# Kernel optimization log

Measured on AMD Instinct MI355X. Metric: run time of the kernel, lower is better.

## Reference

```python
import jax, jax.numpy as jnp
import numpy as np

B, S, E, H = 8, 1024, 1024, 16
D = E // H  # 64
HALF = D // 2  # 32


def _apply_rope(t, freqs):
    # t: (B, S, H, D), freqs: (S, HALF)
    emb = jnp.concatenate([freqs, freqs], axis=-1)  # (S, D)
    cos = jnp.cos(emb)[None, :, None, :]  # (1, S, 1, D)
    sin = jnp.sin(emb)[None, :, None, :]
    t1, t2 = t[..., :D // 2], t[..., D // 2:]
    rot = jnp.concatenate([-t2, t1], axis=-1)
    return t * cos + rot * sin


def setup_inputs() -> dict:
    key = jax.random.key(0)
    ks = jax.random.split(key, 10)
    std = 1.0 / np.sqrt(E)
    return {
        "hidden_states": jax.random.normal(ks[0], (B, S, E), jnp.float32),
        "rotary_pos_emb": jax.random.uniform(ks[1], (S, HALF), jnp.float32) * 10.0,
        "wq": jax.random.normal(ks[2], (E, E), jnp.float32) * std,
        "bq": jnp.zeros((E,), jnp.float32),
        "wk": jax.random.normal(ks[3], (E, E), jnp.float32) * std,
        "bk": jnp.zeros((E,), jnp.float32),
        "wv": jax.random.normal(ks[4], (E, E), jnp.float32) * std,
        "bv": jnp.zeros((E,), jnp.float32),
        "wo": jax.random.normal(ks[5], (E, E), jnp.float32) * std,
        "bo": jnp.zeros((E,), jnp.float32),
    }


def reference(hidden_states, rotary_pos_emb, wq, bq, wk, bk, wv, bv, wo, bo):
    b, s, e = hidden_states.shape
    # QKV projections -> (B, S, H, D)
    q = (hidden_states @ wq + bq).reshape(b, s, H, D)
    k = (hidden_states @ wk + bk).reshape(b, s, H, D)
    v = (hidden_states @ wv + bv).reshape(b, s, H, D)
    # rotary embedding (computed in fp32, matching the torch code)
    q = _apply_rope(q.astype(jnp.float32), rotary_pos_emb).astype(hidden_states.dtype)
    k = _apply_rope(k.astype(jnp.float32), rotary_pos_emb).astype(hidden_states.dtype)
    scale = 1.0 / np.sqrt(D)
    # attention scores (B, H, Sq, Sk)
    scores = jnp.einsum("bqhd,bkhd->bhqk", q, k) * scale
    attn = jax.nn.softmax(scores, axis=-1)
    out = jnp.einsum("bhqk,bkhd->bqhd", attn, v).reshape(b, s, e)
    return out @ wo + bo
```

## Files before the change

kernel.cpp:

```cpp
#include <hip/hip_runtime.h>
#include <hip/hip_bf16.h>

typedef __hip_bfloat16 bf16;
typedef __attribute__((ext_vector_type(8))) short bfrag;
typedef __attribute__((ext_vector_type(4))) float f32x4;

#define MFMA(a, b, c) __builtin_amdgcn_mfma_f32_16x16x32_bf16((a), (b), (c), 0, 0, 0)

__device__ __forceinline__ void async16(const void* g, void* l) {
  __builtin_amdgcn_global_load_lds(
      (const __attribute__((address_space(1))) unsigned int*)g,
      (__attribute__((address_space(3))) unsigned int*)l, 16, 0, 0);
}

__device__ __forceinline__ bfrag ldfrag(const bf16* p) { return *(const bfrag*)p; }

__device__ __forceinline__ unsigned short f2b(float f) {
  return __hip_bfloat16_raw(__float2bfloat16(f)).x;
}
__device__ __forceinline__ float b2f(short u) {
  __hip_bfloat16_raw r; r.x = (unsigned short)u;
  return __bfloat162float(__hip_bfloat16(r));
}

__device__ __forceinline__ bfrag scale8(bfrag x) {
  bfrag y;
#pragma unroll
  for (int i = 0; i < 8; i++) y[i] = (short)f2b(b2f(x[i]) * 0.125f);
  return y;
}

__device__ __forceinline__ void pack4_store(bf16* p, f32x4 v, float s) {
  union { unsigned short h[4]; uint2 u; } pk;
#pragma unroll
  for (int i = 0; i < 4; i++) pk.h[i] = f2b(v[i] * s);
  *(uint2*)p = pk.u;
}


__global__ void k_tables(const float* __restrict__ rp, float* __restrict__ ctab,
                         float* __restrict__ stab) {
  int i = blockIdx.x * 256 + threadIdx.x;
  float f = rp[i];
  ctab[i] = cosf(f);
  stab[i] = sinf(f);
}

__global__ void k_convert_x(const float* __restrict__ X, unsigned short* __restrict__ Xb) {
  int i = blockIdx.x * 256 + threadIdx.x;
  float4 v = *(const float4*)(X + (size_t)i * 4);
  union { unsigned short h[4]; uint2 u; } pk;
  pk.h[0] = f2b(v.x); pk.h[1] = f2b(v.y); pk.h[2] = f2b(v.z); pk.h[3] = f2b(v.w);
  *(uint2*)(Xb + (size_t)i * 4) = pk.u;
}

__global__ void k_transpose_w(const float* __restrict__ wq, const float* __restrict__ wk,
                              const float* __restrict__ wv, const float* __restrict__ wo,
                              unsigned short* __restrict__ tq, unsigned short* __restrict__ tk,
                              unsigned short* __restrict__ tv, unsigned short* __restrict__ to) {
  const int z = blockIdx.z;
  const float* src = (z == 0) ? wq : (z == 1) ? wk : (z == 2) ? wv : wo;
  unsigned short* dst = (z == 0) ? tq : (z == 1) ? tk : (z == 2) ? tv : to;
  const int cc = blockIdx.x * 256 + threadIdx.x;
  const int r0 = blockIdx.y * 8;
  union { unsigned short h[8]; uint4 u; } pk;
#pragma unroll
  for (int i = 0; i < 8; i++) pk.h[i] = f2b(src[(r0 + i) * 1024 + cc]);
  *(uint4*)(dst + cc * 1024 + r0) = pk.u;
}


template <bool ROPE, bool F32OUT, bool BIAS_ROW, int CSTRIDE>
__device__ __forceinline__ void gemm_core(int m0, int n0, const bf16* __restrict__ A,
                                          const bf16* __restrict__ BT,
                                          const float* __restrict__ bias,
                                          bf16* __restrict__ C, float* __restrict__ Cf,
                                          const float* __restrict__ ctab,
                                          const float* __restrict__ stab) {
  __shared__ __align__(16) bf16 As[128 * 32];
  __shared__ __align__(16) bf16 Bs[128 * 32];
  const int tid = threadIdx.x;
  const int w = tid >> 6, l = tid & 63;
  const int wm = (w >> 1) << 6, wn = (w & 1) << 6;
  const int c = l & 15, quad = l >> 4;

  f32x4 acc[4][4] = {};

  const int srow = (w * 2) * 16 + (l >> 2);
  const int scol = (l & 3) * 8;
  const bf16* gA0 = A + (size_t)(m0 + srow) * 1024 + scol;
  const bf16* gA1 = gA0 + 16 * 1024;
  const bf16* gB0 = BT + (size_t)(n0 + srow) * 1024 + scol;
  const bf16* gB1 = gB0 + 16 * 1024;
  char* lA0 = (char*)As + (w * 2) * 1024;
  char* lB0 = (char*)Bs + (w * 2) * 1024;

  for (int k0 = 0; k0 < 1024; k0 += 32) {
    __syncthreads();
    async16(gA0 + k0, lA0);
    async16(gA1 + k0, lA0 + 1024);
    async16(gB0 + k0, lB0);
    async16(gB1 + k0, lB0 + 1024);
    __syncthreads();
    bfrag a[4], b[4];
#pragma unroll
    for (int i = 0; i < 4; i++) a[i] = ldfrag(&As[(wm + i * 16 + c) * 32 + quad * 8]);
#pragma unroll
    for (int j = 0; j < 4; j++) b[j] = ldfrag(&Bs[(wn + j * 16 + c) * 32 + quad * 8]);
#pragma unroll
    for (int i = 0; i < 4; i++)
#pragma unroll
      for (int j = 0; j < 4; j++) acc[i][j] = MFMA(a[i], b[j], acc[i][j]);
  }

#pragma unroll
  for (int i = 0; i < 4; i++) {
    const int mb = m0 + wm + i * 16 + quad * 4;
    if (!ROPE) {
      float brow[4];
      if (BIAS_ROW) {
#pragma unroll
        for (int r = 0; r < 4; r++) brow[r] = bias[mb + r];
      }
#pragma unroll
      for (int j = 0; j < 4; j++) {
        const int n = n0 + wn + j * 16 + c;
        const float bcol = BIAS_ROW ? 0.0f : bias[n];
#pragma unroll
        for (int r = 0; r < 4; r++) {
          const float val = acc[i][j][r] + (BIAS_ROW ? brow[r] : bcol);
          if (F32OUT)
            Cf[(size_t)(mb + r) * CSTRIDE + n] = val;
          else
            C[(size_t)(mb + r) * CSTRIDE + n] = __float2bfloat16(val);
        }
      }
    } else {
#pragma unroll
      for (int j = 0; j < 2; j++) {
        const int n1 = n0 + wn + j * 16 + c;
        const int n2 = n1 + 32;
        const int dl = j * 16 + c;
        const float b1 = bias[n1];
        const float b2 = bias[n2];
#pragma unroll
        for (int r = 0; r < 4; r++) {
          const int m = mb + r;
          const int s = m & 1023;
          const float cs = ctab[s * 32 + dl];
          const float sn = stab[s * 32 + dl];
          const float t1 = acc[i][j][r] + b1;
          const float t2 = acc[i][j + 2][r] + b2;
          C[(size_t)m * CSTRIDE + n1] = __float2bfloat16(t1 * cs - t2 * sn);
          C[(size_t)m * CSTRIDE + n2] = __float2bfloat16(t2 * cs + t1 * sn);
        }
      }
    }
  }
}

__global__ __launch_bounds__(256) void k_gemm_qkv(
    const bf16* __restrict__ X, const bf16* __restrict__ wqT, const bf16* __restrict__ wkT,
    const bf16* __restrict__ wvT, const float* __restrict__ bq, const float* __restrict__ bk,
    const float* __restrict__ bv, const float* __restrict__ ctab,
    const float* __restrict__ stab, bf16* __restrict__ Q, bf16* __restrict__ Kb,
    bf16* __restrict__ VT) {
  const int z = blockIdx.z;
  if (z == 0)
    gemm_core<true, false, false, 1024>(blockIdx.x * 128, blockIdx.y * 128, X, wqT, bq, Q,
                                        nullptr, ctab, stab);
  else if (z == 1)
    gemm_core<true, false, false, 1024>(blockIdx.x * 128, blockIdx.y * 128, X, wkT, bk, Kb,
                                        nullptr, ctab, stab);
  else
    gemm_core<false, false, true, 8192>(blockIdx.y * 128, blockIdx.x * 128, wvT, X, bv, VT,
                                        nullptr, nullptr, nullptr);
}

__global__ __launch_bounds__(256) void k_gemm_o(const bf16* __restrict__ A,
                                                const bf16* __restrict__ BT,
                                                const float* __restrict__ bias,
                                                float* __restrict__ Cf) {
  gemm_core<false, true, false, 1024>(blockIdx.x * 128, blockIdx.y * 128, A, BT, bias,
                                      nullptr, Cf, nullptr, nullptr);
}


__global__ __launch_bounds__(256, 4) void k_flash(const bf16* __restrict__ Q,
                                                  const bf16* __restrict__ K,
                                                  const bf16* __restrict__ VT,
                                                  bf16* __restrict__ O) {
  __shared__ __align__(16) bf16 Ks[64 * 64];
  __shared__ __align__(16) bf16 Vs[64 * 64];
  __shared__ __align__(16) bf16 Ps[4][32 * 72];
  const int qt = blockIdx.x, bh = blockIdx.y;
  const int b = bh >> 4, h = bh & 15;
  const int tid = threadIdx.x, w = tid >> 6, l = tid & 63;
  const int c = l & 15, quad = l >> 4;
  const int c7 = c & 7;

  bfrag qf[2][2];
#pragma unroll
  for (int qs = 0; qs < 2; qs++) {
    const bf16* qp =
        Q + (size_t)(b * 1024 + qt * 128 + w * 32 + qs * 16 + c) * 1024 + h * 64 + quad * 8;
    qf[qs][0] = scale8(ldfrag(qp));
    qf[qs][1] = scale8(ldfrag(qp + 32));
  }

  bfrag onesf;
#pragma unroll
  for (int i = 0; i < 8; i++) onesf[i] = (short)0x3F80;

  f32x4 oacc[2][4] = {};
  f32x4 lacc[2] = {};

  const int sr = l >> 3, scc = l & 7;
  const int swz = (scc ^ sr) * 8;
  const bf16* gK0 = K + (size_t)(b * 1024 + w * 16 + sr) * 1024 + h * 64 + swz;
  const bf16* gV0 = VT + (size_t)(h * 64 + w * 16 + sr) * 8192 + b * 1024 + swz;
  char* lK = (char*)Ks + w * 2048;
  char* lV = (char*)Vs + w * 2048;
  bf16* psw = Ps[w];

  for (int kt = 0; kt < 16; kt++) {
    __syncthreads();
    async16(gK0 + (size_t)(kt * 64) * 1024, lK);
    async16(gK0 + (size_t)(kt * 64 + 8) * 1024, lK + 1024);
    async16(gV0 + kt * 64, lV);
    async16(gV0 + 8 * 8192 + kt * 64, lV + 1024);
    __syncthreads();

#pragma unroll
    for (int qs = 0; qs < 2; qs++) {
      f32x4 sacc[4] = {};
#pragma unroll
      for (int mj = 0; mj < 4; mj++) {
        bfrag k0 = ldfrag(&Ks[(mj * 16 + c) * 64 + (quad ^ c7) * 8]);
        bfrag k1 = ldfrag(&Ks[(mj * 16 + c) * 64 + ((quad + 4) ^ c7) * 8]);
        sacc[mj] = MFMA(k0, qf[qs][0], sacc[mj]);
        sacc[mj] = MFMA(k1, qf[qs][1], sacc[mj]);
      }
      const int psrow = (qs * 16 + c) * 72;
#pragma unroll
      for (int mj = 0; mj < 4; mj++) {
        f32x4 p;
#pragma unroll
        for (int r = 0; r < 4; r++) p[r] = __expf(sacc[mj][r]);
        pack4_store(&psw[psrow + mj * 16 + quad * 4], p, 1.0f);
      }
    }

    bfrag pf[2][2];
#pragma unroll
    for (int qs = 0; qs < 2; qs++) {
      pf[qs][0] = ldfrag(&psw[(qs * 16 + c) * 72 + quad * 8]);
      pf[qs][1] = ldfrag(&psw[(qs * 16 + c) * 72 + 32 + quad * 8]);
      lacc[qs] = MFMA(onesf, pf[qs][0], lacc[qs]);
      lacc[qs] = MFMA(onesf, pf[qs][1], lacc[qs]);
    }
#pragma unroll
    for (int dj = 0; dj < 4; dj++) {
      bfrag v0 = ldfrag(&Vs[(dj * 16 + c) * 64 + (quad ^ c7) * 8]);
      bfrag v1 = ldfrag(&Vs[(dj * 16 + c) * 64 + ((quad + 4) ^ c7) * 8]);
#pragma unroll
      for (int qs = 0; qs < 2; qs++) {
        oacc[qs][dj] = MFMA(v0, pf[qs][0], oacc[qs][dj]);
        oacc[qs][dj] = MFMA(v1, pf[qs][1], oacc[qs][dj]);
      }
    }
  }

#pragma unroll
  for (int qs = 0; qs < 2; qs++) {
    const float inv = 1.0f / lacc[qs][0];
    bf16* op =
        O + (size_t)(b * 1024 + qt * 128 + w * 32 + qs * 16 + c) * 1024 + h * 64 + quad * 4;
#pragma unroll
    for (int dj = 0; dj < 4; dj++) pack4_store(op + dj * 16, oacc[qs][dj], inv);
  }
}


extern "C" void kernel_launch(void* const* d_in, const int* in_sizes, int n_in,
                              void* d_out, int out_size, void* d_ws, size_t ws_size,
                              hipStream_t stream) {
  const float* X  = (const float*)d_in[0];
  const float* rp = (const float*)d_in[1];
  const float* wq = (const float*)d_in[2];
  const float* bq = (const float*)d_in[3];
  const float* wk = (const float*)d_in[4];
  const float* bk = (const float*)d_in[5];
  const float* wv = (const float*)d_in[6];
  const float* bv = (const float*)d_in[7];
  const float* wo = (const float*)d_in[8];
  const float* bo = (const float*)d_in[9];
  float* out = (float*)d_out;

  char* ws = (char*)d_ws;
  const size_t MB = 1024 * 1024;
  bf16* Xb  = (bf16*)(ws + 0 * MB);
  bf16* Q   = (bf16*)(ws + 16 * MB);
  bf16* Kb  = (bf16*)(ws + 32 * MB);
  bf16* VT  = (bf16*)(ws + 48 * MB);
  bf16* O   = (bf16*)(ws + 64 * MB);
  bf16* wqT = (bf16*)(ws + 80 * MB);
  bf16* wkT = (bf16*)(ws + 82 * MB);
  bf16* wvT = (bf16*)(ws + 84 * MB);
  bf16* woT = (bf16*)(ws + 86 * MB);
  float* ctab = (float*)(ws + 88 * MB);
  float* stab = ctab + 1024 * 32;

  k_tables<<<dim3(128), dim3(256), 0, stream>>>(rp, ctab, stab);
  k_convert_x<<<dim3(8192), dim3(256), 0, stream>>>(X, (unsigned short*)Xb);
  k_transpose_w<<<dim3(4, 128, 4), dim3(256), 0, stream>>>(
      wq, wk, wv, wo, (unsigned short*)wqT, (unsigned short*)wkT, (unsigned short*)wvT,
      (unsigned short*)woT);
  k_gemm_qkv<<<dim3(64, 8, 3), dim3(256), 0, stream>>>(Xb, wqT, wkT, wvT, bq, bk, bv, ctab,
                                                       stab, Q, Kb, VT);
  k_flash<<<dim3(8, 128), dim3(256), 0, stream>>>(Q, Kb, VT, O);
  k_gemm_o<<<dim3(64, 8, 1), dim3(256), 0, stream>>>(O, woT, bo, out);
}
```

Measured before the change: 257.3 us.

## Deepen GEMM K-tile to 64 with XOR-swizzled LDS and tile weight transpose

New measurement: 244.7 us. 1.05x faster.

```diff
diff --git a/kernel.cpp b/kernel.cpp
--- a/kernel.cpp
+++ b/kernel.cpp
@@ -58,59 +58,77 @@
                               const float* __restrict__ wv, const float* __restrict__ wo,
                               unsigned short* __restrict__ tq, unsigned short* __restrict__ tk,
                               unsigned short* __restrict__ tv, unsigned short* __restrict__ to) {
+  __shared__ unsigned short T[64][72];
   const int z = blockIdx.z;
   const float* src = (z == 0) ? wq : (z == 1) ? wk : (z == 2) ? wv : wo;
   unsigned short* dst = (z == 0) ? tq : (z == 1) ? tk : (z == 2) ? tv : to;
-  const int cc = blockIdx.x * 256 + threadIdx.x;
-  const int r0 = blockIdx.y * 8;
-  union { unsigned short h[8]; uint4 u; } pk;
-#pragma unroll
-  for (int i = 0; i < 8; i++) pk.h[i] = f2b(src[(r0 + i) * 1024 + cc]);
-  *(uint4*)(dst + cc * 1024 + r0) = pk.u;
+  const int k0 = blockIdx.y * 64, n0 = blockIdx.x * 64;
+  const int t = threadIdx.x;
+  const int kr = t >> 4;
+  const int nc = (t & 15) * 4;
+#pragma unroll
+  for (int g = 0; g < 4; g++) {
+    float4 v = *(const float4*)(src + (size_t)(k0 + g * 16 + kr) * 1024 + n0 + nc);
+    const int kk = g * 16 + kr;
+    T[nc + 0][kk] = f2b(v.x);
+    T[nc + 1][kk] = f2b(v.y);
+    T[nc + 2][kk] = f2b(v.z);
+    T[nc + 3][kk] = f2b(v.w);
+  }
+  __syncthreads();
+  const int nr = t >> 2;
+  const int kc = (t & 3) * 16;
+  unsigned short* dp = dst + (size_t)(n0 + nr) * 1024 + k0 + kc;
+  *(uint4*)(dp + 0) = *(const uint4*)(&T[nr][kc + 0]);
+  *(uint4*)(dp + 8) = *(const uint4*)(&T[nr][kc + 8]);
 }
 
 
 template <bool ROPE, bool F32OUT, bool BIAS_ROW, int CSTRIDE>
-__device__ __forceinline__ void gemm_core(int m0, int n0, const bf16* __restrict__ A,
+__device__ __forceinline__ void gemm_core(bf16* As, bf16* Bs, int m0, int n0,
+                                          const bf16* __restrict__ A,
                                           const bf16* __restrict__ BT,
                                           const float* __restrict__ bias,
                                           bf16* __restrict__ C, float* __restrict__ Cf,
                                           const float* __restrict__ ctab,
                                           const float* __restrict__ stab) {
-  __shared__ __align__(16) bf16 As[128 * 32];
-  __shared__ __align__(16) bf16 Bs[128 * 32];
   const int tid = threadIdx.x;
   const int w = tid >> 6, l = tid & 63;
   const int wm = (w >> 1) << 6, wn = (w & 1) << 6;
   const int c = l & 15, quad = l >> 4;
+  const int c7 = c & 7;
 
   f32x4 acc[4][4] = {};
 
-  const int srow = (w * 2) * 16 + (l >> 2);
-  const int scol = (l & 3) * 8;
-  const bf16* gA0 = A + (size_t)(m0 + srow) * 1024 + scol;
-  const bf16* gA1 = gA0 + 16 * 1024;
-  const bf16* gB0 = BT + (size_t)(n0 + srow) * 1024 + scol;
-  const bf16* gB1 = gB0 + 16 * 1024;
-  char* lA0 = (char*)As + (w * 2) * 1024;
-  char* lB0 = (char*)Bs + (w * 2) * 1024;
-
-  for (int k0 = 0; k0 < 1024; k0 += 32) {
+  const int rl = l >> 3, ch = l & 7;
+  const int sc = ((ch ^ rl) * 8);
+  const bf16* gA = A + (size_t)(m0 + w * 32 + rl) * 1024 + sc;
+  const bf16* gB = BT + (size_t)(n0 + w * 32 + rl) * 1024 + sc;
+  char* lA = (char*)As + w * 32 * 128;
+  char* lB = (char*)Bs + w * 32 * 128;
+
+  for (int k0 = 0; k0 < 1024; k0 += 64) {
     __syncthreads();
-    async16(gA0 + k0, lA0);
-    async16(gA1 + k0, lA0 + 1024);
-    async16(gB0 + k0, lB0);
-    async16(gB1 + k0, lB0 + 1024);
+#pragma unroll
+    for (int g = 0; g < 4; g++) {
+      async16(gA + (size_t)g * 8 * 1024 + k0, lA + g * 1024);
+      async16(gB + (size_t)g * 8 * 1024 + k0, lB + g * 1024);
+    }
     __syncthreads();
-    bfrag a[4], b[4];
-#pragma unroll
-    for (int i = 0; i < 4; i++) a[i] = ldfrag(&As[(wm + i * 16 + c) * 32 + quad * 8]);
-#pragma unroll
-    for (int j = 0; j < 4; j++) b[j] = ldfrag(&Bs[(wn + j * 16 + c) * 32 + quad * 8]);
-#pragma unroll
-    for (int i = 0; i < 4; i++)
-#pragma unroll
-      for (int j = 0; j < 4; j++) acc[i][j] = MFMA(a[i], b[j], acc[i][j]);
+#pragma unroll
+    for (int ks = 0; ks < 2; ks++) {
+      bfrag a[4], b[4];
+#pragma unroll
+      for (int i = 0; i < 4; i++)
+        a[i] = ldfrag(&As[(wm + i * 16 + c) * 64 + (((ks * 4 + quad) ^ c7) * 8)]);
+#pragma unroll
+      for (int j = 0; j < 4; j++)
+        b[j] = ldfrag(&Bs[(wn + j * 16 + c) * 64 + (((ks * 4 + quad) ^ c7) * 8)]);
+#pragma unroll
+      for (int i = 0; i < 4; i++)
+#pragma unroll
+        for (int j = 0; j < 4; j++) acc[i][j] = MFMA(a[i], b[j], acc[i][j]);
+    }
   }
 
 #pragma unroll
@@ -165,24 +183,28 @@
     const float* __restrict__ bv, const float* __restrict__ ctab,
     const float* __restrict__ stab, bf16* __restrict__ Q, bf16* __restrict__ Kb,
     bf16* __restrict__ VT) {
+  __shared__ __align__(16) bf16 As[128 * 64];
+  __shared__ __align__(16) bf16 Bs[128 * 64];
   const int z = blockIdx.z;
   if (z == 0)
-    gemm_core<true, false, false, 1024>(blockIdx.x * 128, blockIdx.y * 128, X, wqT, bq, Q,
-                                        nullptr, ctab, stab);
+    gemm_core<true, false, false, 1024>(As, Bs, blockIdx.x * 128, blockIdx.y * 128, X, wqT,
+                                        bq, Q, nullptr, ctab, stab);
   else if (z == 1)
-    gemm_core<true, false, false, 1024>(blockIdx.x * 128, blockIdx.y * 128, X, wkT, bk, Kb,
-                                        nullptr, ctab, stab);
+    gemm_core<true, false, false, 1024>(As, Bs, blockIdx.x * 128, blockIdx.y * 128, X, wkT,
+                                        bk, Kb, nullptr, ctab, stab);
   else
-    gemm_core<false, false, true, 8192>(blockIdx.y * 128, blockIdx.x * 128, wvT, X, bv, VT,
-                                        nullptr, nullptr, nullptr);
+    gemm_core<false, false, true, 8192>(As, Bs, blockIdx.y * 128, blockIdx.x * 128, wvT, X,
+                                        bv, VT, nullptr, nullptr, nullptr);
 }
 
 __global__ __launch_bounds__(256) void k_gemm_o(const bf16* __restrict__ A,
                                                 const bf16* __restrict__ BT,
                                                 const float* __restrict__ bias,
                                                 float* __restrict__ Cf) {
-  gemm_core<false, true, false, 1024>(blockIdx.x * 128, blockIdx.y * 128, A, BT, bias,
-                                      nullptr, Cf, nullptr, nullptr);
+  __shared__ __align__(16) bf16 As[128 * 64];
+  __shared__ __align__(16) bf16 Bs[128 * 64];
+  gemm_core<false, true, false, 1024>(As, Bs, blockIdx.x * 128, blockIdx.y * 128, A, BT,
+                                      bias, nullptr, Cf, nullptr, nullptr);
 }
 
 
@@ -313,7 +335,7 @@
 
   k_tables<<<dim3(128), dim3(256), 0, stream>>>(rp, ctab, stab);
   k_convert_x<<<dim3(8192), dim3(256), 0, stream>>>(X, (unsigned short*)Xb);
-  k_transpose_w<<<dim3(4, 128, 4), dim3(256), 0, stream>>>(
+  k_transpose_w<<<dim3(16, 16, 4), dim3(256), 0, stream>>>(
       wq, wk, wv, wo, (unsigned short*)wqT, (unsigned short*)wkT, (unsigned short*)wvT,
       (unsigned short*)woT);
   k_gemm_qkv<<<dim3(64, 8, 3), dim3(256), 0, stream>>>(Xb, wqT, wkT, wvT, bq, bk, bv, ctab,
```
